# Performance work log

Hardware: AMD Instinct MI355X
Metric: run time of the kernel (lower is better)

The kernel has to match this reference:

```python
import jax, jax.numpy as jnp
import numpy as np

B, S, H, D = 2, 2048, 16, 64
HID = H * D
NEG = -1e9


def _rope(q, cos, sin):
    # q: (B,S,H,D); cos/sin: (S, D//2) -> broadcast (1,S,1,D//2)
    qe, qo = q[..., 0::2], q[..., 1::2]
    c = cos[None, :, None, :]
    s = sin[None, :, None, :]
    oe = qe * c - qo * s
    oo = qe * s + qo * c
    return jnp.stack([oe, oo], axis=-1).reshape(q.shape)  # interleave even/odd pairs


def setup_inputs() -> dict:
    key = jax.random.key(0)
    ks = jax.random.split(key, 9)
    scale = 1.0 / np.sqrt(HID)
    x = jax.random.normal(ks[0], (B, S, HID), jnp.float32)
    Wq = jax.random.normal(ks[1], (HID, HID), jnp.float32) * scale
    Wk = jax.random.normal(ks[2], (HID, HID), jnp.float32) * scale
    Wv = jax.random.normal(ks[3], (HID, HID), jnp.float32) * scale
    Wo = jax.random.normal(ks[4], (HID, HID), jnp.float32) * scale
    bq = jnp.zeros((HID,), jnp.float32)
    bk = jnp.zeros((HID,), jnp.float32)
    bv = jnp.zeros((HID,), jnp.float32)
    bo = jnp.zeros((HID,), jnp.float32)
    # standard RoPE angles: theta_i = 10000^{-2i/D}
    inv_freq = 1.0 / (10000.0 ** (np.arange(0, D, 2, dtype=np.float32) / D))  # (D/2,)
    angles = jnp.arange(S, dtype=jnp.float32)[:, None] * jnp.asarray(inv_freq)[None, :]
    freqs_cos = jnp.cos(angles)
    freqs_sin = jnp.sin(angles)
    causal = jnp.tril(jnp.ones((S, S), bool))
    mask = jnp.where(causal, 0.0, NEG).astype(jnp.float32)[None, None]  # (1,1,S,S)
    return dict(x=x, Wq=Wq, bq=bq, Wk=Wk, bk=bk, Wv=Wv, bv=bv, Wo=Wo, bo=bo,
                mask=mask, freqs_cos=freqs_cos, freqs_sin=freqs_sin)


def reference(x, Wq, bq, Wk, bk, Wv, bv, Wo, bo, mask, freqs_cos, freqs_sin):
    b, s, hid = x.shape
    # weights stored (in, out): y = x @ W + b (equivalent to torch Linear with W^T)
    q = (x @ Wq + bq).reshape(b, s, H, D)
    k = (x @ Wk + bk).reshape(b, s, H, D)
    v = (x @ Wv + bv).reshape(b, s, H, D)
    q = _rope(q, freqs_cos, freqs_sin)
    k = _rope(k, freqs_cos, freqs_sin)
    q = q.transpose(0, 2, 1, 3)  # (B,H,S,D)
    k = k.transpose(0, 2, 1, 3)
    v = v.transpose(0, 2, 1, 3)
    scores = jnp.einsum('bhqd,bhkd->bhqk', q, k) / np.sqrt(D)
    scores = scores + mask
    attn = jax.nn.softmax(scores.astype(jnp.float32), axis=-1)
    out = jnp.einsum('bhqk,bhkd->bhqd', attn, v)
    out = out.transpose(0, 2, 1, 3).reshape(b, s, hid)
    return out @ Wo + bo
```

## Files before the change

### kernel.cpp

```cpp
#include <hip/hip_runtime.h>
#include <hip/hip_bf16.h>

#define BDIM 2
#define SDIM 2048
#define HDIM 16
#define DDIM 64
#define HID  1024
#define MDIM (BDIM * SDIM)

typedef __attribute__((ext_vector_type(8))) short short8;
typedef __attribute__((ext_vector_type(4))) short short4v;
typedef __attribute__((ext_vector_type(4))) float f32x4;
typedef __attribute__((ext_vector_type(2))) unsigned int uint2v;

__device__ __forceinline__ float bf2f(short u) {
    union { unsigned int i; float f; } x;
    x.i = ((unsigned int)(unsigned short)u) << 16;
    return x.f;
}
__device__ __forceinline__ short f2bf(float f) {
    union { float f; unsigned int i; } x; x.f = f;
    unsigned int r = x.i + 0x7fffu + ((x.i >> 16) & 1u);
    return (short)(r >> 16);
}
__device__ __forceinline__ unsigned int cvtpk_bf16(float lo, float hi) {
    unsigned int r;
    asm("v_cvt_pk_bf16_f32 %0, %1, %2" : "=v"(r) : "v"(lo), "v"(hi));
    return r;
}
__device__ __forceinline__ int swz(int row, int c8) {
    return row * 64 + ((c8 ^ (row & 7)) << 3);
}

__global__ __launch_bounds__(256) void cvt_bf16(const float* __restrict__ in,
                                               short* __restrict__ out, int n) {
    int i = (blockIdx.x * 256 + threadIdx.x) * 8;
    if (i >= n) return;
    float4 a = *(const float4*)(in + i);
    float4 b = *(const float4*)(in + i + 4);
    short8 v;
    v[0] = f2bf(a.x); v[1] = f2bf(a.y); v[2] = f2bf(a.z); v[3] = f2bf(a.w);
    v[4] = f2bf(b.x); v[5] = f2bf(b.y); v[6] = f2bf(b.z); v[7] = f2bf(b.w);
    *(short8*)(out + i) = v;
}

__global__ __launch_bounds__(256) void transpose4(
    const float* __restrict__ w0, const float* __restrict__ w1,
    const float* __restrict__ w2, const float* __restrict__ w3,
    short* __restrict__ o0, short* __restrict__ o1,
    short* __restrict__ o2, short* __restrict__ o3)
{
    const float* src; short* dst;
    int z = blockIdx.z;
    if (z == 0)      { src = w0; dst = o0; }
    else if (z == 1) { src = w1; dst = o1; }
    else if (z == 2) { src = w2; dst = o2; }
    else             { src = w3; dst = o3; }
    __shared__ float t[64][65];
    int r0 = blockIdx.y * 64, c0 = blockIdx.x * 64;
    int rd_r = threadIdx.x >> 4, rd_c = (threadIdx.x & 15) * 4;
    #pragma unroll
    for (int it = 0; it < 4; it++) {
        int rr = rd_r + it * 16;
        float4 v = *(const float4*)(src + (size_t)(r0 + rr) * HID + c0 + rd_c);
        t[rr][rd_c + 0] = v.x; t[rr][rd_c + 1] = v.y;
        t[rr][rd_c + 2] = v.z; t[rr][rd_c + 3] = v.w;
    }
    __syncthreads();
    int or_ = threadIdx.x >> 3, oc8 = (threadIdx.x & 7) * 8;
    #pragma unroll
    for (int half = 0; half < 2; half++) {
        int dr = or_ + half * 32;
        short8 v;
        #pragma unroll
        for (int i = 0; i < 8; i++) v[i] = f2bf(t[oc8 + i][dr]);
        *(short8*)(dst + (size_t)(c0 + dr) * HID + r0 + oc8) = v;
    }
}

__global__ __launch_bounds__(256) void gemm_bf16(
    const short* __restrict__ X,
    const short* __restrict__ Wt0,
    const float* __restrict__ b0, const float* __restrict__ b1, const float* __restrict__ b2,
    const float* __restrict__ cosb, const float* __restrict__ sinb,
    short* __restrict__ out0, float* __restrict__ outf,
    int modeBase)
{
    constexpr int LDK = 40;
    __shared__ __align__(16) short Asm[2][128 * LDK];
    __shared__ __align__(16) short Bsm[2][128 * LDK];
    int z = blockIdx.z;
    int mode = modeBase + z;
    const short* Wt = Wt0 + (size_t)z * HID * HID;
    const float* bias = (z == 0) ? b0 : (z == 1) ? b1 : b2;
    short* outp = out0 + (size_t)z * MDIM * HID;

    int tid = threadIdx.x;
    int lane = tid & 63, wave = tid >> 6;
    int wr = wave >> 1, wc = wave & 1;
    int m0 = blockIdx.x * 128, n0 = blockIdx.y * 128;
    int sr = tid >> 2, sc = (tid & 3) * 8;
    int lr = lane & 15, lg = lane >> 4;

    const short* ax = X  + (size_t)(m0 + sr) * HID + sc;
    const short* bx = Wt + (size_t)(n0 + sr) * HID + sc;
    int wA = sr * LDK + sc, wA2 = (sr + 64) * LDK + sc;

    f32x4 acc[4][4] = {};
    constexpr int NK = HID / 32;

    short8 a0, a1, b0v, b1v;
    a0  = *(const short8*)(ax);
    a1  = *(const short8*)(ax + (size_t)64 * HID);
    b0v = *(const short8*)(bx);
    b1v = *(const short8*)(bx + (size_t)64 * HID);
    *(short8*)(Asm[0] + wA)  = a0;
    *(short8*)(Asm[0] + wA2) = a1;
    *(short8*)(Bsm[0] + wA)  = b0v;
    *(short8*)(Bsm[0] + wA2) = b1v;
    a0  = *(const short8*)(ax + 32);
    a1  = *(const short8*)(ax + (size_t)64 * HID + 32);
    b0v = *(const short8*)(bx + 32);
    b1v = *(const short8*)(bx + (size_t)64 * HID + 32);

    int cur = 0;
    for (int ki = 0; ki < NK; ki++) {
        __syncthreads();
        if (ki + 1 < NK) {
            *(short8*)(Asm[cur ^ 1] + wA)  = a0;
            *(short8*)(Asm[cur ^ 1] + wA2) = a1;
            *(short8*)(Bsm[cur ^ 1] + wA)  = b0v;
            *(short8*)(Bsm[cur ^ 1] + wA2) = b1v;
        }
        if (ki + 2 < NK) {
            int k0 = (ki + 2) * 32;
            a0  = *(const short8*)(ax + k0);
            a1  = *(const short8*)(ax + (size_t)64 * HID + k0);
            b0v = *(const short8*)(bx + k0);
            b1v = *(const short8*)(bx + (size_t)64 * HID + k0);
        }
        short8 af[4], bfr[4];
        #pragma unroll
        for (int m = 0; m < 4; m++)
            af[m] = *(const short8*)(Asm[cur] + (wr * 64 + m * 16 + lr) * LDK + lg * 8);
        #pragma unroll
        for (int n = 0; n < 4; n++)
            bfr[n] = *(const short8*)(Bsm[cur] + (wc * 64 + n * 16 + lr) * LDK + lg * 8);
        __builtin_amdgcn_s_setprio(1);
        #pragma unroll
        for (int m = 0; m < 4; m++)
            #pragma unroll
            for (int n = 0; n < 4; n++)
                acc[m][n] = __builtin_amdgcn_mfma_f32_16x16x32_bf16(af[m], bfr[n], acc[m][n], 0, 0, 0);
        __builtin_amdgcn_s_setprio(0);
        cur ^= 1;
    }

    #pragma unroll
    for (int m = 0; m < 4; m++) {
        #pragma unroll
        for (int n = 0; n < 4; n++) {
            int gr0 = m0 + wr * 64 + m * 16 + lg * 4;
            int gc  = n0 + wc * 64 + n * 16 + lr;
            if (mode == 3) {
                #pragma unroll
                for (int j = 0; j < 4; j++)
                    outf[(size_t)(gr0 + j) * HID + gc] = acc[m][n][j] + bias[gc];
            } else if (mode == 2) {
                int bb = gr0 >> 11, s0 = gr0 & (SDIM - 1);
                int h = gc >> 6, dd = gc & 63;
                short4v pk;
                #pragma unroll
                for (int j = 0; j < 4; j++) pk[j] = f2bf(acc[m][n][j] + bias[gc]);
                *(short4v*)(outp + ((size_t)((bb * HDIM + h) * DDIM + dd)) * SDIM + s0) = pk;
            } else {
                #pragma unroll
                for (int j = 0; j < 4; j++) {
                    int gr = gr0 + j;
                    int bb = gr >> 11, s = gr & (SDIM - 1);
                    int h = gc >> 6, dd = gc & 63;
                    float v = acc[m][n][j] + bias[gc];
                    float p  = __shfl_xor(v, 1);
                    float cc = cosb[s * 32 + (dd >> 1)];
                    float ss = sinb[s * 32 + (dd >> 1)];
                    v = (dd & 1) ? (p * ss + v * cc) : (v * cc - p * ss);
                    outp[((size_t)((bb * HDIM + h) * SDIM + s)) * DDIM + dd] = f2bf(v);
                }
            }
        }
    }
}

__global__ __launch_bounds__(256) void attn_fwd(
    const short* __restrict__ Q,
    const short* __restrict__ K,
    const short* __restrict__ Vt,
    short* __restrict__ O)
{
    __shared__ __align__(16) short Ks0[64 * 64], Ks1[64 * 64];
    __shared__ __align__(16) short Vs0[64 * 64], Vs1[64 * 64];
    __shared__ __align__(16) short Ps[4][16 * 64];
    int bx = blockIdx.x;
    int qA = bx, qB = 31 - bx;
    int bh = blockIdx.y;
    int tid = threadIdx.x;
    int lane = tid & 63, wave = tid >> 6;
    int lr = lane & 15, lg = lane >> 4;
    const short* qbase  = Q  + ((size_t)bh * SDIM) * DDIM;
    const short* kbase  = K  + ((size_t)bh * SDIM) * DDIM;
    const short* vtbase = Vt + ((size_t)bh * DDIM) * SDIM;

    const float SCALE = 0.125f * 1.44269504088896340736f;

    int rowA = qA * 64 + wave * 16 + lr;
    int rowB = qB * 64 + wave * 16 + lr;
    short8 qfA[2], qfB[2];
    #pragma unroll
    for (int ks = 0; ks < 2; ks++) {
        short8 a = *(const short8*)(qbase + (size_t)rowA * DDIM + ks * 32 + lg * 8);
        short8 b = *(const short8*)(qbase + (size_t)rowB * DDIM + ks * 32 + lg * 8);
        short8 ra, rb;
        #pragma unroll
        for (int i = 0; i < 8; i++) {
            ra[i] = f2bf(bf2f(a[i]) * SCALE);
            rb[i] = f2bf(bf2f(b[i]) * SCALE);
        }
        qfA[ks] = ra; qfB[ks] = rb;
    }

    float mA = -1e30f, lA = 0.f, mB = -1e30f, lB = 0.f;
    f32x4 oaccA[4] = {}, oaccB[4] = {};

    int sr_ = tid >> 3, sc8 = tid & 7;
    int vd_ = tid >> 2, vc8 = (tid & 3) * 2;
    int kw0 = swz(sr_, sc8), kw1 = swz(sr_ + 32, sc8);
    int vw0 = swz(vd_, vc8), vw1 = swz(vd_, vc8 + 1);
    int fo[8];
    #pragma unroll
    for (int ks = 0; ks < 2; ks++)
        #pragma unroll
        for (int n = 0; n < 4; n++) fo[ks * 4 + n] = swz(n * 16 + lr, ks * 4 + lg);
    int po[2] = { swz(lr, lg), swz(lr, 4 + lg) };
    int pw[4];
    #pragma unroll
    for (int n = 0; n < 4; n++)
        pw[n] = lr * 64 + (((n * 2 + (lg >> 1)) ^ (lr & 7)) << 3) + (lg & 1) * 4;

    int nt = qB + 1;

    short8 kreg0, kreg1, vreg0, vreg1;
    kreg0 = *(const short8*)(kbase + (size_t)sr_ * DDIM + sc8 * 8);
    kreg1 = *(const short8*)(kbase + (size_t)(sr_ + 32) * DDIM + sc8 * 8);
    vreg0 = *(const short8*)(vtbase + (size_t)vd_ * SDIM + vc8 * 8);
    vreg1 = *(const short8*)(vtbase + (size_t)vd_ * SDIM + vc8 * 8 + 8);
    *(short8*)(Ks0 + kw0) = kreg0;
    *(short8*)(Ks0 + kw1) = kreg1;
    *(short8*)(Vs0 + vw0) = vreg0;
    *(short8*)(Vs0 + vw1) = vreg1;
    kreg0 = *(const short8*)(kbase + (size_t)(64 + sr_) * DDIM + sc8 * 8);
    kreg1 = *(const short8*)(kbase + (size_t)(96 + sr_) * DDIM + sc8 * 8);
    vreg0 = *(const short8*)(vtbase + (size_t)vd_ * SDIM + 64 + vc8 * 8);
    vreg1 = *(const short8*)(vtbase + (size_t)vd_ * SDIM + 64 + vc8 * 8 + 8);
    const short* kpre = kbase + (size_t)(128 + sr_) * DDIM + sc8 * 8;
    const short* vpre = vtbase + (size_t)vd_ * SDIM + 128 + vc8 * 8;

    auto sm_pv = [&](f32x4 (&st)[4], float& m_run, float& l_run, f32x4 (&oacc)[4],
                     int qrow_, bool diag, int kt, short* VsC) {
        if (diag) {
            #pragma unroll
            for (int n = 0; n < 4; n++)
                #pragma unroll
                for (int j = 0; j < 4; j++) {
                    int k = kt * 64 + n * 16 + lg * 4 + j;
                    if (k > qrow_) st[n][j] = -1e30f;
                }
        }
        float m4[4], s4[4];
        #pragma unroll
        for (int n = 0; n < 4; n++)
            m4[n] = fmaxf(fmaxf(st[n][0], st[n][1]), fmaxf(st[n][2], st[n][3]));
        float mx = fmaxf(fmaxf(m4[0], m4[1]), fmaxf(m4[2], m4[3]));
        mx = fmaxf(mx, __shfl_xor(mx, 16));
        mx = fmaxf(mx, __shfl_xor(mx, 32));
        float mnew;
        if (__any(mx > m_run + 8.f)) {
            mnew = fmaxf(m_run, mx);
            float scl = exp2f(m_run - mnew);
            l_run *= scl;
            float rescl[4];
            #pragma unroll
            for (int j = 0; j < 4; j++)
                rescl[j] = __int_as_float(__builtin_amdgcn_ds_bpermute((lg * 4 + j) * 4, __float_as_int(scl)));
            #pragma unroll
            for (int n = 0; n < 4; n++)
                #pragma unroll
                for (int j = 0; j < 4; j++) oacc[n][j] *= rescl[j];
            m_run = mnew;
        } else {
            mnew = m_run;
        }
        #pragma unroll
        for (int n = 0; n < 4; n++) {
            #pragma unroll
            for (int j = 0; j < 4; j++) st[n][j] = exp2f(st[n][j] - mnew);
            s4[n] = (st[n][0] + st[n][1]) + (st[n][2] + st[n][3]);
        }
        float ls = (s4[0] + s4[1]) + (s4[2] + s4[3]);
        ls += __shfl_xor(ls, 16);
        ls += __shfl_xor(ls, 32);
        l_run += ls;
        #pragma unroll
        for (int n = 0; n < 4; n++) {
            uint2v pk;
            pk[0] = cvtpk_bf16(st[n][0], st[n][1]);
            pk[1] = cvtpk_bf16(st[n][2], st[n][3]);
            *(uint2v*)(Ps[wave] + pw[n]) = pk;
        }
        __builtin_amdgcn_s_setprio(1);
        #pragma unroll
        for (int ks = 0; ks < 2; ks++) {
            short8 pf = *(const short8*)(Ps[wave] + po[ks]);
            #pragma unroll
            for (int n = 0; n < 4; n++) {
                short8 vf = *(const short8*)(VsC + fo[ks * 4 + n]);
                oacc[n] = __builtin_amdgcn_mfma_f32_16x16x32_bf16(pf, vf, oacc[n], 0, 0, 0);
            }
        }
        __builtin_amdgcn_s_setprio(0);
    };

    auto tile = [&](int kt, short* KsC, short* VsC, short* KsN, short* VsN) {
        __syncthreads();
        if (kt + 1 < nt) {
            *(short8*)(KsN + kw0) = kreg0;
            *(short8*)(KsN + kw1) = kreg1;
            *(short8*)(VsN + vw0) = vreg0;
            *(short8*)(VsN + vw1) = vreg1;
        }
        if (kt + 2 < nt) {
            kreg0 = *(const short8*)(kpre);
            kreg1 = *(const short8*)(kpre + 32 * DDIM);
            vreg0 = *(const short8*)(vpre);
            vreg1 = *(const short8*)(vpre + 8);
        }
        kpre += 64 * DDIM;
        vpre += 64;

        bool actA = (kt <= qA);
        f32x4 stA[4] = {}, stB[4] = {};
        __builtin_amdgcn_s_setprio(1);
        #pragma unroll
        for (int ks = 0; ks < 2; ks++) {
            short8 kf[4];
            #pragma unroll
            for (int n = 0; n < 4; n++) kf[n] = *(const short8*)(KsC + fo[ks * 4 + n]);
            #pragma unroll
            for (int n = 0; n < 4; n++)
                stB[n] = __builtin_amdgcn_mfma_f32_16x16x32_bf16(kf[n], qfB[ks], stB[n], 0, 0, 0);
            if (actA)
                #pragma unroll
                for (int n = 0; n < 4; n++)
                    stA[n] = __builtin_amdgcn_mfma_f32_16x16x32_bf16(kf[n], qfA[ks], stA[n], 0, 0, 0);
        }
        __builtin_amdgcn_s_setprio(0);
        if (actA) sm_pv(stA, mA, lA, oaccA, rowA, kt == qA, kt, VsC);
        sm_pv(stB, mB, lB, oaccB, rowB, kt == qB, kt, VsC);
    };

    for (int kt = 0; kt < nt; kt += 2) {
        tile(kt, Ks0, Vs0, Ks1, Vs1);
        if (kt + 1 < nt) tile(kt + 1, Ks1, Vs1, Ks0, Vs0);
    }

    int b = bh >> 4, h = bh & 15;
    auto epi = [&](f32x4 (&oacc)[4], float l_run, int qb_) {
        float linv[4];
        #pragma unroll
        for (int j = 0; j < 4; j++)
            linv[j] = 1.f / __int_as_float(__builtin_amdgcn_ds_bpermute((lg * 4 + j) * 4, __float_as_int(l_run)));
        #pragma unroll
        for (int n = 0; n < 4; n++)
            #pragma unroll
            for (int j = 0; j < 4; j++) {
                int s = qb_ * 64 + wave * 16 + lg * 4 + j;
                int dd = n * 16 + lr;
                O[(((size_t)(b * SDIM + s) * HDIM) + h) * DDIM + dd] = f2bf(oacc[n][j] * linv[j]);
            }
    };
    epi(oaccA, lA, qA);
    epi(oaccB, lB, qB);
}

extern "C" void kernel_launch(void* const* d_in, const int* in_sizes, int n_in,
                              void* d_out, int out_size, void* d_ws, size_t ws_size,
                              hipStream_t stream) {
    const float* x  = (const float*)d_in[0];
    const float* Wq = (const float*)d_in[1];
    const float* bq = (const float*)d_in[2];
    const float* Wk = (const float*)d_in[3];
    const float* bk = (const float*)d_in[4];
    const float* Wv = (const float*)d_in[5];
    const float* bv = (const float*)d_in[6];
    const float* Wo = (const float*)d_in[7];
    const float* bo = (const float*)d_in[8];
    const float* fc = (const float*)d_in[10];
    const float* fs = (const float*)d_in[11];
    float* out = (float*)d_out;
    short* ws  = (short*)d_ws;

    const size_t MM = (size_t)HID * HID;
    short* xb     = ws;
    short* wt_qkv = ws + 4 * MM;
    short* wot    = ws + 7 * MM;
    short* qt     = ws + 8 * MM;
    short* ktb    = ws + 12 * MM;
    short* vtb    = ws + 16 * MM;
    short* ao     = ws + 20 * MM;

    cvt_bf16<<<dim3((MDIM * HID) / (256 * 8)), 256, 0, stream>>>(x, xb, MDIM * HID);
    transpose4<<<dim3(16, 16, 4), 256, 0, stream>>>(Wq, Wk, Wv, Wo,
                                                    wt_qkv, wt_qkv + MM, wt_qkv + 2 * MM, wot);
    gemm_bf16<<<dim3(MDIM / 128, HID / 128, 3), 256, 0, stream>>>(
        xb, wt_qkv, bq, bk, bv, fc, fs, qt, nullptr, 0);
    attn_fwd<<<dim3(16, BDIM * HDIM), 256, 0, stream>>>(qt, ktb, vtb, ao);
    gemm_bf16<<<dim3(MDIM / 128, HID / 128, 1), 256, 0, stream>>>(
        ao, wot, bo, bo, bo, fc, fs, nullptr, out, 3);
}
```

Baseline: 125.7 us.

## Split paired causal query tiles across two wave groups with 512-thread attention blocks

The attention kernel now launches 512 threads per block. Waves 0-3 handle the long query tile qB and waves 4-7 handle the short tile qA, where before every wave processed both tiles in sequence. The K/V staging is spread over all 512 threads, one 16-byte load each instead of two. The aim is to double the waves per CU and halve each wave's serial work and register pressure. In exchange, the qA group sits idle once its causal range ends, and barriers now span 8 waves.

```diff
diff --git a/kernel.cpp b/kernel.cpp
--- a/kernel.cpp
+++ b/kernel.cpp
@@ -191,7 +191,7 @@
     }
 }
 
-__global__ __launch_bounds__(256) void attn_fwd(
+__global__ __launch_bounds__(512) void attn_fwd(
     const short* __restrict__ Q,
     const short* __restrict__ K,
     const short* __restrict__ Vt,
@@ -199,12 +199,13 @@
 {
     __shared__ __align__(16) short Ks0[64 * 64], Ks1[64 * 64];
     __shared__ __align__(16) short Vs0[64 * 64], Vs1[64 * 64];
-    __shared__ __align__(16) short Ps[4][16 * 64];
+    __shared__ __align__(16) short Ps[8][16 * 64];
     int bx = blockIdx.x;
     int qA = bx, qB = 31 - bx;
     int bh = blockIdx.y;
     int tid = threadIdx.x;
     int lane = tid & 63, wave = tid >> 6;
+    int wv = wave & 3, grp = wave >> 2;
     int lr = lane & 15, lg = lane >> 4;
     const short* qbase  = Q  + ((size_t)bh * SDIM) * DDIM;
     const short* kbase  = K  + ((size_t)bh * SDIM) * DDIM;
@@ -212,29 +213,24 @@
 
     const float SCALE = 0.125f * 1.44269504088896340736f;
 
-    int rowA = qA * 64 + wave * 16 + lr;
-    int rowB = qB * 64 + wave * 16 + lr;
-    short8 qfA[2], qfB[2];
+    int qt_own = grp ? qA : qB;
+    int qrow = qt_own * 64 + wv * 16 + lr;
+
+    short8 qf[2];
     #pragma unroll
     for (int ks = 0; ks < 2; ks++) {
-        short8 a = *(const short8*)(qbase + (size_t)rowA * DDIM + ks * 32 + lg * 8);
-        short8 b = *(const short8*)(qbase + (size_t)rowB * DDIM + ks * 32 + lg * 8);
-        short8 ra, rb;
-        #pragma unroll
-        for (int i = 0; i < 8; i++) {
-            ra[i] = f2bf(bf2f(a[i]) * SCALE);
-            rb[i] = f2bf(bf2f(b[i]) * SCALE);
-        }
-        qfA[ks] = ra; qfB[ks] = rb;
-    }
-
-    float mA = -1e30f, lA = 0.f, mB = -1e30f, lB = 0.f;
-    f32x4 oaccA[4] = {}, oaccB[4] = {};
+        short8 a = *(const short8*)(qbase + (size_t)qrow * DDIM + ks * 32 + lg * 8);
+        short8 ra;
+        #pragma unroll
+        for (int i = 0; i < 8; i++) ra[i] = f2bf(bf2f(a[i]) * SCALE);
+        qf[ks] = ra;
+    }
+
+    float m_run = -1e30f, l_run = 0.f;
+    f32x4 oacc[4] = {};
 
     int sr_ = tid >> 3, sc8 = tid & 7;
-    int vd_ = tid >> 2, vc8 = (tid & 3) * 2;
-    int kw0 = swz(sr_, sc8), kw1 = swz(sr_ + 32, sc8);
-    int vw0 = swz(vd_, vc8), vw1 = swz(vd_, vc8 + 1);
+    int kw = swz(sr_, sc8);
     int fo[8];
     #pragma unroll
     for (int ks = 0; ks < 2; ks++)
@@ -248,31 +244,24 @@
 
     int nt = qB + 1;
 
-    short8 kreg0, kreg1, vreg0, vreg1;
-    kreg0 = *(const short8*)(kbase + (size_t)sr_ * DDIM + sc8 * 8);
-    kreg1 = *(const short8*)(kbase + (size_t)(sr_ + 32) * DDIM + sc8 * 8);
-    vreg0 = *(const short8*)(vtbase + (size_t)vd_ * SDIM + vc8 * 8);
-    vreg1 = *(const short8*)(vtbase + (size_t)vd_ * SDIM + vc8 * 8 + 8);
-    *(short8*)(Ks0 + kw0) = kreg0;
-    *(short8*)(Ks0 + kw1) = kreg1;
-    *(short8*)(Vs0 + vw0) = vreg0;
-    *(short8*)(Vs0 + vw1) = vreg1;
-    kreg0 = *(const short8*)(kbase + (size_t)(64 + sr_) * DDIM + sc8 * 8);
-    kreg1 = *(const short8*)(kbase + (size_t)(96 + sr_) * DDIM + sc8 * 8);
-    vreg0 = *(const short8*)(vtbase + (size_t)vd_ * SDIM + 64 + vc8 * 8);
-    vreg1 = *(const short8*)(vtbase + (size_t)vd_ * SDIM + 64 + vc8 * 8 + 8);
+    short8 kreg, vreg;
+    kreg = *(const short8*)(kbase + (size_t)sr_ * DDIM + sc8 * 8);
+    vreg = *(const short8*)(vtbase + (size_t)sr_ * SDIM + sc8 * 8);
+    *(short8*)(Ks0 + kw) = kreg;
+    *(short8*)(Vs0 + kw) = vreg;
+    kreg = *(const short8*)(kbase + (size_t)(64 + sr_) * DDIM + sc8 * 8);
+    vreg = *(const short8*)(vtbase + (size_t)sr_ * SDIM + 64 + sc8 * 8);
     const short* kpre = kbase + (size_t)(128 + sr_) * DDIM + sc8 * 8;
-    const short* vpre = vtbase + (size_t)vd_ * SDIM + 128 + vc8 * 8;
-
-    auto sm_pv = [&](f32x4 (&st)[4], float& m_run, float& l_run, f32x4 (&oacc)[4],
-                     int qrow_, bool diag, int kt, short* VsC) {
+    const short* vpre = vtbase + (size_t)sr_ * SDIM + 128 + sc8 * 8;
+
+    auto sm_pv = [&](f32x4 (&st)[4], bool diag, int kt, short* VsC) {
         if (diag) {
             #pragma unroll
             for (int n = 0; n < 4; n++)
                 #pragma unroll
                 for (int j = 0; j < 4; j++) {
                     int k = kt * 64 + n * 16 + lg * 4 + j;
-                    if (k > qrow_) st[n][j] = -1e30f;
+                    if (k > qrow) st[n][j] = -1e30f;
                 }
         }
         float m4[4], s4[4];
@@ -332,39 +321,32 @@
     auto tile = [&](int kt, short* KsC, short* VsC, short* KsN, short* VsN) {
         __syncthreads();
         if (kt + 1 < nt) {
-            *(short8*)(KsN + kw0) = kreg0;
-            *(short8*)(KsN + kw1) = kreg1;
-            *(short8*)(VsN + vw0) = vreg0;
-            *(short8*)(VsN + vw1) = vreg1;
+            *(short8*)(KsN + kw) = kreg;
+            *(short8*)(VsN + kw) = vreg;
         }
         if (kt + 2 < nt) {
-            kreg0 = *(const short8*)(kpre);
-            kreg1 = *(const short8*)(kpre + 32 * DDIM);
-            vreg0 = *(const short8*)(vpre);
-            vreg1 = *(const short8*)(vpre + 8);
+            kreg = *(const short8*)(kpre);
+            vreg = *(const short8*)(vpre);
         }
         kpre += 64 * DDIM;
         vpre += 64;
 
-        bool actA = (kt <= qA);
-        f32x4 stA[4] = {}, stB[4] = {};
-        __builtin_amdgcn_s_setprio(1);
-        #pragma unroll
-        for (int ks = 0; ks < 2; ks++) {
-            short8 kf[4];
-            #pragma unroll
-            for (int n = 0; n < 4; n++) kf[n] = *(const short8*)(KsC + fo[ks * 4 + n]);
-            #pragma unroll
-            for (int n = 0; n < 4; n++)
-                stB[n] = __builtin_amdgcn_mfma_f32_16x16x32_bf16(kf[n], qfB[ks], stB[n], 0, 0, 0);
-            if (actA)
+        bool act = grp ? (kt <= qA) : true;
+        if (act) {
+            f32x4 st[4] = {};
+            __builtin_amdgcn_s_setprio(1);
+            #pragma unroll
+            for (int ks = 0; ks < 2; ks++) {
+                short8 kf[4];
+                #pragma unroll
+                for (int n = 0; n < 4; n++) kf[n] = *(const short8*)(KsC + fo[ks * 4 + n]);
                 #pragma unroll
                 for (int n = 0; n < 4; n++)
-                    stA[n] = __builtin_amdgcn_mfma_f32_16x16x32_bf16(kf[n], qfA[ks], stA[n], 0, 0, 0);
-        }
-        __builtin_amdgcn_s_setprio(0);
-        if (actA) sm_pv(stA, mA, lA, oaccA, rowA, kt == qA, kt, VsC);
-        sm_pv(stB, mB, lB, oaccB, rowB, kt == qB, kt, VsC);
+                    st[n] = __builtin_amdgcn_mfma_f32_16x16x32_bf16(kf[n], qf[ks], st[n], 0, 0, 0);
+            }
+            __builtin_amdgcn_s_setprio(0);
+            sm_pv(st, kt == qt_own, kt, VsC);
+        }
     };
 
     for (int kt = 0; kt < nt; kt += 2) {
@@ -373,22 +355,18 @@
     }
 
     int b = bh >> 4, h = bh & 15;
-    auto epi = [&](f32x4 (&oacc)[4], float l_run, int qb_) {
-        float linv[4];
-        #pragma unroll
-        for (int j = 0; j < 4; j++)
-            linv[j] = 1.f / __int_as_float(__builtin_amdgcn_ds_bpermute((lg * 4 + j) * 4, __float_as_int(l_run)));
-        #pragma unroll
-        for (int n = 0; n < 4; n++)
-            #pragma unroll
-            for (int j = 0; j < 4; j++) {
-                int s = qb_ * 64 + wave * 16 + lg * 4 + j;
-                int dd = n * 16 + lr;
-                O[(((size_t)(b * SDIM + s) * HDIM) + h) * DDIM + dd] = f2bf(oacc[n][j] * linv[j]);
-            }
-    };
-    epi(oaccA, lA, qA);
-    epi(oaccB, lB, qB);
+    float linv[4];
+    #pragma unroll
+    for (int j = 0; j < 4; j++)
+        linv[j] = 1.f / __int_as_float(__builtin_amdgcn_ds_bpermute((lg * 4 + j) * 4, __float_as_int(l_run)));
+    #pragma unroll
+    for (int n = 0; n < 4; n++)
+        #pragma unroll
+        for (int j = 0; j < 4; j++) {
+            int s = qt_own * 64 + wv * 16 + lg * 4 + j;
+            int dd = n * 16 + lr;
+            O[(((size_t)(b * SDIM + s) * HDIM) + h) * DDIM + dd] = f2bf(oacc[n][j] * linv[j]);
+        }
 }
 
 extern "C" void kernel_launch(void* const* d_in, const int* in_sizes, int n_in,
@@ -422,7 +400,7 @@
                                                     wt_qkv, wt_qkv + MM, wt_qkv + 2 * MM, wot);
     gemm_bf16<<<dim3(MDIM / 128, HID / 128, 3), 256, 0, stream>>>(
         xb, wt_qkv, bq, bk, bv, fc, fs, qt, nullptr, 0);
-    attn_fwd<<<dim3(16, BDIM * HDIM), 256, 0, stream>>>(qt, ktb, vtb, ao);
+    attn_fwd<<<dim3(16, BDIM * HDIM), 512, 0, stream>>>(qt, ktb, vtb, ao);
     gemm_bf16<<<dim3(MDIM / 128, HID / 128, 1), 256, 0, stream>>>(
         ao, wot, bo, bo, bo, fc, fs, nullptr, out, 3);
 }
```

Result: faster. 118.1 us (-6.0%).
